# Optimization experiments

Measured on AMD Instinct MI355X. Metric: run time of the kernel, lower is better.

The kernel has to match this reference:

```python
import jax, jax.numpy as jnp
import numpy as np

B = 16384
F = 128   # num_features
H = 128   # hidden_dim
E = 32    # embedding_dim


def setup_inputs() -> dict:
    key = jax.random.key(0)
    k_x, k_w1, k_b1, k_w2, k_b2 = jax.random.split(key, 5)
    # Per-feature params stacked along feature axis.
    # Layer 1: Linear(1 -> H): weight [F, H] (in_dim==1 squeezed), bias [F, H]
    # Layer 2: Linear(H -> E): weight [F, H, E], bias [F, E]
    # Torch default init: U(-1/sqrt(fan_in), 1/sqrt(fan_in))
    w1 = jax.random.uniform(k_w1, (F, H), jnp.float32, -1.0, 1.0)          # fan_in=1
    b1 = jax.random.uniform(k_b1, (F, H), jnp.float32, -1.0, 1.0)
    bound2 = 1.0 / np.sqrt(H)
    w2 = jax.random.uniform(k_w2, (F, H, E), jnp.float32, -bound2, bound2)
    b2 = jax.random.uniform(k_b2, (F, E), jnp.float32, -bound2, bound2)
    x = jax.random.normal(k_x, (B, F), jnp.float32)
    return {"x": x, "w1": w1, "b1": b1, "w2": w2, "b2": b2}


def reference(x, w1, b1, w2, b2):
    # Fused over features: broadcast-mul replaces K=1 matmuls,
    # single batched GEMM replaces per-feature second Linear.
    h = jax.nn.relu(x[:, :, None] * w1[None] + b1[None])   # [B, F, H]
    out = jnp.einsum('bfh,fhe->bfe', h, w2) + b2[None]      # [B, F, E]
    return out.reshape(x.shape[0], F * E)                   # concat along last dim
```

## Files before the change

kernel.cpp:

```cpp
#include <hip/hip_runtime.h>
#include <math.h>

#define B_N 16384
#define F_N 128
#define H_N 128
#define E_N 32
#define ROWS (H_N + 1)

typedef float f4v __attribute__((ext_vector_type(4)));

__device__ __forceinline__ int eidxA(int e) { return ((e >> 2) << 3) | (e & 3); }

__global__ __launch_bounds__(128) void build_tables(
    const float* __restrict__ w1, const float* __restrict__ b1,
    const float* __restrict__ w2, const float* __restrict__ b2,
    float* __restrict__ ts_out, float* __restrict__ tab)
{
    __shared__ float w1s[H_N], b1s[H_N], ts[H_N];
    __shared__ int   hidx[H_N];
    __shared__ float w2s[H_N * E_N];
    __shared__ float dA[H_N * E_N];
    __shared__ float dC[H_N * E_N];
    __shared__ float baseA[4 * E_N], baseC[4 * E_N];
    __shared__ float gtA[4 * E_N], gtC[4 * E_N];

    const int f   = blockIdx.x;
    const int tid = threadIdx.x;

    float w1v = w1[f * H_N + tid];
    float b1v = b1[f * H_N + tid];
    w1s[tid] = w1v;
    b1s[tid] = b1v;
    ts[tid]   = (w1v != 0.0f) ? (-b1v / w1v) : INFINITY;
    hidx[tid] = tid;

    {
        const float4* src = (const float4*)(w2 + (size_t)f * H_N * E_N);
        float4*       dst = (float4*)w2s;
        #pragma unroll
        for (int it = 0; it < 8; ++it) dst[it * 128 + tid] = src[it * 128 + tid];
    }
    __syncthreads();

    for (int k = 2; k <= H_N; k <<= 1) {
        for (int j = k >> 1; j > 0; j >>= 1) {
            int ixj = tid ^ j;
            if (ixj > tid) {
                float a = ts[tid], bv = ts[ixj];
                bool up = ((tid & k) == 0);
                bool sw = up ? (a > bv) : (a < bv);
                if (sw) {
                    int ia = hidx[tid];
                    ts[tid] = bv; ts[ixj] = a;
                    hidx[tid] = hidx[ixj]; hidx[ixj] = ia;
                }
            }
            __syncthreads();
        }
    }

    ts_out[f * H_N + tid] = ts[tid];

    const int e = tid & 31;
    const int g = tid >> 5;

    #pragma unroll 4
    for (int jj = 0; jj < 32; ++jj) {
        int   j   = g * 32 + jj;
        int   p   = hidx[j];
        float w1h = w1s[p], b1h = b1s[p];
        float w2v = w2s[p * E_N + e];
        float s   = (w1h > 0.f) ? 1.f : ((w1h < 0.f) ? -1.f : 0.f);
        dA[j * E_N + e] = s * w1h * w2v;
        dC[j * E_N + e] = s * b1h * w2v;
    }
    {
        float pA = 0.f, pC = 0.f;
        #pragma unroll 4
        for (int hh = 0; hh < 32; ++hh) {
            int   h   = g * 32 + hh;
            float w1h = w1s[h], b1h = b1s[h];
            float w2v = w2s[h * E_N + e];
            if (w1h < 0.f) {
                pA = fmaf(w1h, w2v, pA);
                pC = fmaf(b1h, w2v, pC);
            } else if (w1h == 0.f && b1h > 0.f) {
                pC = fmaf(b1h, w2v, pC);
            }
        }
        baseA[g * E_N + e] = pA;
        baseC[g * E_N + e] = pC;
    }

    {
        float aA = 0.f, aC = 0.f;
        for (int jj = 0; jj < 32; ++jj) {
            int idx = (g * 32 + jj) * E_N + e;
            aA += dA[idx]; dA[idx] = aA;
            aC += dC[idx]; dC[idx] = aC;
        }
        gtA[g * E_N + e] = aA;
        gtC[g * E_N + e] = aC;
    }
    __syncthreads();

    float offA = baseA[e] + baseA[E_N + e] + baseA[2 * E_N + e] + baseA[3 * E_N + e];
    float offC = baseC[e] + baseC[E_N + e] + baseC[2 * E_N + e] + baseC[3 * E_N + e]
               + b2[f * E_N + e];
    for (int gg = 0; gg < g; ++gg) {
        offA += gtA[gg * E_N + e];
        offC += gtC[gg * E_N + e];
    }

    const size_t base = (size_t)f * ROWS * 64;
    const int    eA   = eidxA(e);
    if (g == 0) {
        tab[base + eA]     = offA;
        tab[base + eA + 4] = offC;
    }
    #pragma unroll 4
    for (int jj = 0; jj < 32; ++jj) {
        int j = g * 32 + jj;
        tab[base + (size_t)(j + 1) * 64 + eA]     = offA + dA[j * E_N + e];
        tab[base + (size_t)(j + 1) * 64 + eA + 4] = offC + dC[j * E_N + e];
    }
}

#define FH 16
#define NB 64

__global__ __launch_bounds__(256, 4) void apply_tables(
    const float* __restrict__ x, const float* __restrict__ ts,
    const float* __restrict__ tab, float* __restrict__ out)
{
    __shared__ float          lds_t[FH * ROWS];
    __shared__ float          xs[NB * FH];
    __shared__ unsigned short los[NB * FH];

    const int tid = threadIdx.x;

    const unsigned bid = blockIdx.x;
    const int f0 = (int)(bid & 7u) * FH;
    const int b0 = (int)(bid >> 3) * NB;

    {
        const float4* src = (const float4*)(ts + (size_t)f0 * H_N);
        #pragma unroll
        for (int it = 0; it < 2; ++it) {
            int    vi  = it * 256 + tid;
            float4 v   = src[vi];
            int    idx = vi * 4;
            int    fl_ = idx >> 7;
            int    j   = idx & 127;
            float* dst = &lds_t[fl_ * ROWS + j];
            dst[0] = v.x; dst[1] = v.y; dst[2] = v.z; dst[3] = v.w;
        }
    }
    {
        int bl = tid >> 2;
        int fq = (tid & 3) * 4;
        float4 v = *(const float4*)(x + (size_t)(b0 + bl) * F_N + f0 + fq);
        *(float4*)(&xs[bl * FH + fq]) = v;
    }
    __syncthreads();

    {
        const int fa = tid & 15;
        const int rg = tid >> 4;
        const float* tloc = &lds_t[fa * ROWS];
        float xv[4];
        int   lo[4], hi[4];
        #pragma unroll
        for (int j = 0; j < 4; ++j) {
            xv[j] = xs[(rg * 4 + j) * FH + fa];
            lo[j] = 0; hi[j] = H_N;
        }
        #pragma unroll
        for (int s = 0; s < 7; ++s) {
            #pragma unroll
            for (int j = 0; j < 4; ++j) {
                int  mid = (lo[j] + hi[j]) >> 1;
                bool lt  = tloc[mid] < xv[j];
                lo[j] = lt ? mid + 1 : lo[j];
                hi[j] = lt ? hi[j] : mid;
            }
        }
        #pragma unroll
        for (int j = 0; j < 4; ++j)
            los[(rg * 4 + j) * FH + fa] = (unsigned short)lo[j];
    }
    __syncthreads();

    const int fl = (tid >> 3) & 15;
    const int eq = tid & 7;
    const int bh = tid >> 7;
    const int rbase = bh * 32;
    const f4v* tb = (const f4v*)(tab + (size_t)(f0 + fl) * ROWS * 64 + eq * 8);
    float*     op = out + (size_t)(b0 + rbase) * (F_N * E_N)
                        + (size_t)(f0 + fl) * E_N + eq * 4;

    #pragma unroll
    for (int c = 0; c < 4; ++c) {
        float xv[8];
        f4v   a[8], cc[8];
        #pragma unroll
        for (int j = 0; j < 8; ++j) {
            int r  = c * 8 + j;
            int lo = los[(rbase + r) * FH + fl];
            xv[j]  = xs[(rbase + r) * FH + fl];
            a[j]   = tb[lo * 16];
            cc[j]  = tb[lo * 16 + 1];
        }
        #pragma unroll
        for (int j = 0; j < 8; ++j) {
            f4v o;
            o.x = fmaf(xv[j], a[j].x, cc[j].x);
            o.y = fmaf(xv[j], a[j].y, cc[j].y);
            o.z = fmaf(xv[j], a[j].z, cc[j].z);
            o.w = fmaf(xv[j], a[j].w, cc[j].w);
            __builtin_nontemporal_store(
                o, (f4v*)(op + (size_t)(c * 8 + j) * (F_N * E_N)));
        }
    }
}

__global__ __launch_bounds__(256) void direct_kernel(
    const float* __restrict__ x, const float* __restrict__ w1,
    const float* __restrict__ b1, const float* __restrict__ w2,
    const float* __restrict__ b2, float* __restrict__ out)
{
    __shared__ float w1s[H_N], b1s[H_N], b2s[E_N];
    __shared__ float w2s[H_N * E_N];
    const int f   = blockIdx.y;
    const int tid = threadIdx.x;
    if (tid < H_N) { w1s[tid] = w1[f * H_N + tid]; b1s[tid] = b1[f * H_N + tid]; }
    for (int i = tid; i < H_N * E_N; i += 256) w2s[i] = w2[(size_t)f * H_N * E_N + i];
    if (tid < E_N) b2s[tid] = b2[f * E_N + tid];
    __syncthreads();

    const int b  = blockIdx.x * 256 + tid;
    float xv = x[(size_t)b * F_N + f];
    float acc[E_N];
    #pragma unroll
    for (int e = 0; e < E_N; ++e) acc[e] = b2s[e];
    for (int h = 0; h < H_N; ++h) {
        float hv = fmaxf(fmaf(xv, w1s[h], b1s[h]), 0.f);
        #pragma unroll
        for (int e = 0; e < E_N; ++e) acc[e] = fmaf(hv, w2s[h * E_N + e], acc[e]);
    }
    float* op = out + (size_t)b * (F_N * E_N) + (size_t)f * E_N;
    #pragma unroll
    for (int e = 0; e < E_N; e += 4)
        *(float4*)(op + e) = make_float4(acc[e], acc[e + 1], acc[e + 2], acc[e + 3]);
}

extern "C" void kernel_launch(void* const* d_in, const int* in_sizes, int n_in,
                              void* d_out, int out_size, void* d_ws, size_t ws_size,
                              hipStream_t stream) {
    const float* x  = (const float*)d_in[0];
    const float* w1 = (const float*)d_in[1];
    const float* b1 = (const float*)d_in[2];
    const float* w2 = (const float*)d_in[3];
    const float* b2 = (const float*)d_in[4];
    float* out = (float*)d_out;

    const size_t n_ts  = (size_t)F_N * H_N;
    const size_t n_tab = (size_t)F_N * ROWS * 64;
    const size_t need  = (n_ts + n_tab) * sizeof(float);

    if (ws_size >= need) {
        float* ts  = (float*)d_ws;
        float* tab = ts + n_ts;
        build_tables<<<dim3(F_N), dim3(128), 0, stream>>>(w1, b1, w2, b2, ts, tab);
        apply_tables<<<dim3((B_N / NB) * (F_N / FH)), dim3(256), 0, stream>>>(x, ts, tab, out);
    } else {
        direct_kernel<<<dim3(B_N / 256, F_N), dim3(256), 0, stream>>>(x, w1, b1, w2, b2, out);
    }
}
```

Before: 293.8 us.

## Tile apply kernel over full feature rows for contiguous output writes

The apply kernel now gives each block 16 batch rows across all 128 features instead of a 64-row by 16-feature tile. Each wavefront writes whole contiguous 2 KB stretches of an output row, which should give the large output store stream better coalescing. In exchange every block loads the full 128x129 breakpoint table into LDS (about 66 KB), so occupancy drops to 2 blocks per CU, and that table load is amortized over only 16 rows.

```diff
diff --git a/kernel.cpp b/kernel.cpp
--- a/kernel.cpp
+++ b/kernel.cpp
@@ -126,27 +126,23 @@
     }
 }
 
-#define FH 16
-#define NB 64
-
-__global__ __launch_bounds__(256, 4) void apply_tables(
+#define NB 16
+
+__global__ __launch_bounds__(256, 2) void apply_tables(
     const float* __restrict__ x, const float* __restrict__ ts,
     const float* __restrict__ tab, float* __restrict__ out)
 {
-    __shared__ float          lds_t[FH * ROWS];
-    __shared__ float          xs[NB * FH];
-    __shared__ unsigned short los[NB * FH];
+    __shared__ float          lds_t[F_N * ROWS];
+    __shared__ float          xs[NB * F_N];
+    __shared__ unsigned short los[NB * F_N];
 
     const int tid = threadIdx.x;
-
-    const unsigned bid = blockIdx.x;
-    const int f0 = (int)(bid & 7u) * FH;
-    const int b0 = (int)(bid >> 3) * NB;
-
-    {
-        const float4* src = (const float4*)(ts + (size_t)f0 * H_N);
-        #pragma unroll
-        for (int it = 0; it < 2; ++it) {
+    const int b0  = blockIdx.x * NB;
+
+    {
+        const float4* src = (const float4*)ts;
+        #pragma unroll
+        for (int it = 0; it < 16; ++it) {
             int    vi  = it * 256 + tid;
             float4 v   = src[vi];
             int    idx = vi * 4;
@@ -157,28 +153,32 @@
         }
     }
     {
-        int bl = tid >> 2;
-        int fq = (tid & 3) * 4;
-        float4 v = *(const float4*)(x + (size_t)(b0 + bl) * F_N + f0 + fq);
-        *(float4*)(&xs[bl * FH + fq]) = v;
-    }
-    __syncthreads();
-
-    {
-        const int fa = tid & 15;
-        const int rg = tid >> 4;
+        #pragma unroll
+        for (int it = 0; it < 2; ++it) {
+            int vi = it * 256 + tid;
+            int bl = vi >> 5;
+            int fq = (vi & 31) * 4;
+            float4 v = *(const float4*)(x + (size_t)(b0 + bl) * F_N + fq);
+            *(float4*)(&xs[bl * F_N + fq]) = v;
+        }
+    }
+    __syncthreads();
+
+    {
+        const int fa = tid & 127;
+        const int rg = tid >> 7;
         const float* tloc = &lds_t[fa * ROWS];
-        float xv[4];
-        int   lo[4], hi[4];
-        #pragma unroll
-        for (int j = 0; j < 4; ++j) {
-            xv[j] = xs[(rg * 4 + j) * FH + fa];
+        float xv[8];
+        int   lo[8], hi[8];
+        #pragma unroll
+        for (int j = 0; j < 8; ++j) {
+            xv[j] = xs[(rg * 8 + j) * F_N + fa];
             lo[j] = 0; hi[j] = H_N;
         }
         #pragma unroll
         for (int s = 0; s < 7; ++s) {
             #pragma unroll
-            for (int j = 0; j < 4; ++j) {
+            for (int j = 0; j < 8; ++j) {
                 int  mid = (lo[j] + hi[j]) >> 1;
                 bool lt  = tloc[mid] < xv[j];
                 lo[j] = lt ? mid + 1 : lo[j];
@@ -186,40 +186,49 @@
             }
         }
         #pragma unroll
-        for (int j = 0; j < 4; ++j)
-            los[(rg * 4 + j) * FH + fa] = (unsigned short)lo[j];
-    }
-    __syncthreads();
-
-    const int fl = (tid >> 3) & 15;
-    const int eq = tid & 7;
-    const int bh = tid >> 7;
-    const int rbase = bh * 32;
-    const f4v* tb = (const f4v*)(tab + (size_t)(f0 + fl) * ROWS * 64 + eq * 8);
-    float*     op = out + (size_t)(b0 + rbase) * (F_N * E_N)
-                        + (size_t)(f0 + fl) * E_N + eq * 4;
+        for (int j = 0; j < 8; ++j)
+            los[(rg * 8 + j) * F_N + fa] = (unsigned short)lo[j];
+    }
+    __syncthreads();
+
+    const int lane = tid & 63;
+    const int wv   = tid >> 6;
+    const int eq   = lane & 7;
+    const int fo   = lane >> 3;
+    const f4v* tbase = (const f4v*)tab + eq * 2;
 
     #pragma unroll
-    for (int c = 0; c < 4; ++c) {
-        float xv[8];
-        f4v   a[8], cc[8];
-        #pragma unroll
-        for (int j = 0; j < 8; ++j) {
-            int r  = c * 8 + j;
-            int lo = los[(rbase + r) * FH + fl];
-            xv[j]  = xs[(rbase + r) * FH + fl];
-            a[j]   = tb[lo * 16];
-            cc[j]  = tb[lo * 16 + 1];
-        }
-        #pragma unroll
-        for (int j = 0; j < 8; ++j) {
-            f4v o;
-            o.x = fmaf(xv[j], a[j].x, cc[j].x);
-            o.y = fmaf(xv[j], a[j].y, cc[j].y);
-            o.z = fmaf(xv[j], a[j].z, cc[j].z);
-            o.w = fmaf(xv[j], a[j].w, cc[j].w);
-            __builtin_nontemporal_store(
-                o, (f4v*)(op + (size_t)(c * 8 + j) * (F_N * E_N)));
+    for (int rr = 0; rr < 4; ++rr) {
+        const int r = wv * 4 + rr;
+        const float*          xrow = &xs[r * F_N];
+        const unsigned short* lrow = &los[r * F_N];
+        float* oprow = out + (size_t)(b0 + r) * (F_N * E_N);
+
+        #pragma unroll
+        for (int kc = 0; kc < 4; ++kc) {
+            float xv[4];
+            f4v   a[4], cc[4];
+            #pragma unroll
+            for (int jk = 0; jk < 4; ++jk) {
+                int k  = kc * 4 + jk;
+                int fl = k * 8 + fo;
+                int lo = lrow[fl];
+                xv[jk] = xrow[fl];
+                const f4v* tp = tbase + (size_t)(fl * ROWS + lo) * 16;
+                a[jk]  = tp[0];
+                cc[jk] = tp[1];
+            }
+            #pragma unroll
+            for (int jk = 0; jk < 4; ++jk) {
+                int k = kc * 4 + jk;
+                f4v o;
+                o.x = fmaf(xv[jk], a[jk].x, cc[jk].x);
+                o.y = fmaf(xv[jk], a[jk].y, cc[jk].y);
+                o.z = fmaf(xv[jk], a[jk].z, cc[jk].z);
+                o.w = fmaf(xv[jk], a[jk].w, cc[jk].w);
+                __builtin_nontemporal_store(
+                    o, (f4v*)(oprow + k * 256 + fo * 32 + eq * 4));
+            }
         }
     }
 }
@@ -272,7 +281,7 @@
         float* ts  = (float*)d_ws;
         float* tab = ts + n_ts;
         build_tables<<<dim3(F_N), dim3(128), 0, stream>>>(w1, b1, w2, b2, ts, tab);
-        apply_tables<<<dim3((B_N / NB) * (F_N / FH)), dim3(256), 0, stream>>>(x, ts, tab, out);
+        apply_tables<<<dim3(B_N / NB), dim3(256), 0, stream>>>(x, ts, tab, out);
     } else {
         direct_kernel<<<dim3(B_N / 256, F_N), dim3(256), 0, stream>>>(x, w1, b1, w2, b2, out);
     }
```

After: 291.3 us. No clear change (-0.9%).
